# Kernel tuning notes

Measured on AMD Instinct MI355X. Metric: run time of the kernel, lower is better.

Reference implementation:

```python
import jax, jax.numpy as jnp
import numpy as np

DIM = 512
NUM_LATENTS = 512
HIDDEN = 48  # PointEmbed sinusoidal embedding dim (divisible by 6)


def make_basis():
    k = HIDDEN // 6
    e = (2.0 ** np.arange(k)) * np.pi
    z = np.zeros(k)
    basis = np.stack([
        np.concatenate([e, z, z]),
        np.concatenate([z, e, z]),
        np.concatenate([z, z, e]),
    ])  # [3, HIDDEN//2]
    return jnp.asarray(basis, jnp.float32)


def layernorm(x, g, b, eps=1e-5):
    m = x.mean(-1, keepdims=True)
    v = ((x - m) ** 2).mean(-1, keepdims=True)
    return (x - m) / jnp.sqrt(v + eps) * g + b


def point_embed(x, basis, w, b):
    # x: [B, N, 3] -> [B, N, DIM//2]
    proj = jnp.einsum('bnd,de->bne', x, basis)
    feat = jnp.concatenate([jnp.sin(proj), jnp.cos(proj), x], axis=-1)  # [B,N,51]
    return feat @ w + b


def fps_single(points, num_samples):
    # deterministic farthest point sampling starting at index 0; non-differentiable
    pts = jax.lax.stop_gradient(points)
    N = pts.shape[0]

    def body(carry, _):
        dists, last = carry
        d = jnp.sum((pts - pts[last]) ** 2, axis=-1)
        dists = jnp.minimum(dists, d)
        nxt = jnp.argmax(dists).astype(jnp.int32)
        return (dists, nxt), nxt

    init = (jnp.full((N,), 1e10, pts.dtype), jnp.int32(0))
    _, idxs = jax.lax.scan(body, init, None, length=num_samples - 1)
    return jnp.concatenate([jnp.zeros((1,), jnp.int32), idxs])


def setup_inputs() -> dict:
    key = jax.random.key(0)
    ks = jax.random.split(key, 16)
    B, T, N, D = 16, 3, 2048, 3
    s = 0.02
    inp = {
        'pc': jax.random.normal(ks[0], (B, T, N, D), jnp.float32),
        'pc2': jax.random.normal(ks[1], (B, T, N, D), jnp.float32),
        'basis': make_basis(),
        'pe_w': jax.random.normal(ks[2], (HIDDEN + 3, DIM // 2), jnp.float32) * s,
        'pe_b': jnp.zeros((DIM // 2,), jnp.float32),
        'lnq_g': jnp.ones((DIM,), jnp.float32), 'lnq_b': jnp.zeros((DIM,), jnp.float32),
        'lnc_g': jnp.ones((DIM,), jnp.float32), 'lnc_b': jnp.zeros((DIM,), jnp.float32),
        'wq': jax.random.normal(ks[3], (DIM, DIM), jnp.float32) * s,
        'wkv': jax.random.normal(ks[4], (DIM, 2 * DIM), jnp.float32) * s,
        'wo': jax.random.normal(ks[5], (DIM, DIM), jnp.float32) * s,
        'bo': jnp.zeros((DIM,), jnp.float32),
        'lnf_g': jnp.ones((DIM,), jnp.float32), 'lnf_b': jnp.zeros((DIM,), jnp.float32),
        'w1': jax.random.normal(ks[6], (DIM, 8 * DIM), jnp.float32) * s,
        'b1': jnp.zeros((8 * DIM,), jnp.float32),
        'w2': jax.random.normal(ks[7], (4 * DIM, DIM), jnp.float32) * s,
        'b2': jnp.zeros((DIM,), jnp.float32),
    }
    return inp


def reference(pc, pc2, basis, pe_w, pe_b, lnq_g, lnq_b, lnc_g, lnc_b,
              wq, wkv, wo, bo, lnf_g, lnf_b, w1, b1, w2, b2):
    B, T, N, D = pc.shape
    # FPS on the first frame, per batch element (batch-local indices)
    idx = jax.vmap(lambda p: fps_single(p, NUM_LATENTS))(pc[:, 0])  # [B, M]
    idx4 = idx[:, None, :, None]  # broadcast over T and D
    sampled = jnp.take_along_axis(pc, idx4, axis=2).reshape(B * T, NUM_LATENTS, D)
    sampled2 = jnp.take_along_axis(pc2, idx4, axis=2).reshape(B * T, NUM_LATENTS, D)
    pcf = pc.reshape(B * T, N, D)
    pcf2 = pc2.reshape(B * T, N, D)

    emb_s = jnp.concatenate([point_embed(sampled, basis, pe_w, pe_b),
                             point_embed(sampled2, basis, pe_w, pe_b)], axis=-1)
    emb_c = jnp.concatenate([point_embed(pcf, basis, pe_w, pe_b),
                             point_embed(pcf2, basis, pe_w, pe_b)], axis=-1)

    # PreNorm cross-attention (1 head, dim_head = DIM)
    q_in = layernorm(emb_s, lnq_g, lnq_b)
    c_in = layernorm(emb_c, lnc_g, lnc_b)
    q = q_in @ wq
    kv = c_in @ wkv
    k, v = jnp.split(kv, 2, axis=-1)
    scale = DIM ** -0.5
    attn = jax.nn.softmax(jnp.einsum('bmd,bnd->bmn', q, k) * scale, axis=-1)
    out = jnp.einsum('bmn,bnd->bmd', attn, v) @ wo + bo
    x = out + emb_s

    # PreNorm GEGLU feed-forward
    h = layernorm(x, lnf_g, lnf_b) @ w1 + b1
    a, g = jnp.split(h, 2, axis=-1)
    x = (a * jax.nn.gelu(g, approximate=False)) @ w2 + b2 + x

    return x.reshape(B, T, NUM_LATENTS, DIM)
```

## Files before the change

### kernel.cpp

```cpp
#include <hip/hip_runtime.h>

#define NB    16
#define NT    3
#define NCTX  2048
#define NLAT  512
#define DIMV  512
#define HALFD 256
#define NFEAT 51
#define NBT   48
#define MROWS 24576
#define GRP   6
#define NGRP  8
#define GROWS 12288
#define FUSED_BLKS (NB + GROWS/16 + 4096)

typedef unsigned short bfu;
typedef short bf16x8 __attribute__((ext_vector_type(8)));
typedef float f32x4  __attribute__((ext_vector_type(4)));
typedef float f32x2  __attribute__((ext_vector_type(2)));

__device__ __forceinline__ float bf2f(bfu u){ return __uint_as_float(((unsigned int)u) << 16); }
__device__ __forceinline__ bfu f2bf(float f){
  unsigned int u = __float_as_uint(f);
  u += 0x7FFFu + ((u >> 16) & 1u);
  return (bfu)(u >> 16);
}
__device__ __forceinline__ float loadE(const float* p){ return *p; }
__device__ __forceinline__ float loadE(const bfu* p){ return bf2f(*p); }
__device__ __forceinline__ void storeE(float* p, float v){ *p = v; }
__device__ __forceinline__ void storeE(bfu* p, float v){ *p = f2bf(v); }
__device__ __forceinline__ bfu to_bfu(float f){ return f2bf(f); }
__device__ __forceinline__ bfu to_bfu(bfu u){ return u; }

#define GLD16(gp, lp) __builtin_amdgcn_global_load_lds(                       \
    (const __attribute__((address_space(1))) unsigned int*)(gp),              \
    (__attribute__((address_space(3))) unsigned int*)(lp), 16, 0, 0)

template<int KSTEP>
__device__ __forceinline__ int swzr(int r){
  constexpr int CPR = KSTEP / 8;
  return (KSTEP == 32) ? ((r >> 1) & 3) : (r & (CPR - 1));
}

#define DPP_ARGMAX_STAGE(CTRL)                                                \
  {                                                                           \
    const int svb = __builtin_amdgcn_update_dpp(vb, vb, CTRL, 0xF, 0xF, false); \
    const int sib = __builtin_amdgcn_update_dpp(ib, ib, CTRL, 0xF, 0xF, false); \
    const float sv = __int_as_float(svb);                                     \
    const float cv = __int_as_float(vb);                                      \
    if (sv > cv || (sv == cv && sib < ib)){ vb = svb; ib = sib; }             \
  }

__device__ __forceinline__ void fps_body(int b, int tid, const float* __restrict__ pc,
                                         int* __restrict__ idx_out,
                                         float4* pts, int (*mbuf)[4]){
  const int lane = tid & 63, w = tid >> 6;
  const int wbase = w << 10;
  const float* src = pc + (size_t)b * (NT * NCTX * 3);

  f32x2 x2[8], y2[8], z2[8], d2[8];
  #pragma unroll
  for (int j = 0; j < 8; ++j){
    #pragma unroll
    for (int h = 0; h < 2; ++h){
      const int p = wbase + ((2 * j + h) << 6) + lane;
      const float xx = src[p * 3 + 0];
      const float yy = src[p * 3 + 1];
      const float zz = src[p * 3 + 2];
      x2[j][h] = xx; y2[j][h] = yy; z2[j][h] = zz;
      pts[p] = make_float4(xx, yy, zz, 0.f);
    }
    d2[j][0] = 1e10f; d2[j][1] = 1e10f;
  }
  if (tid == 0) idx_out[b * NLAT] = 0;
  __syncthreads();

  int last = 0;
  for (int step = 1; step < NLAT; ++step){
    const float4 lp = pts[last];

    #pragma unroll
    for (int j = 0; j < 8; ++j){
      const f32x2 dx = x2[j] - lp.x;
      const f32x2 dy = y2[j] - lp.y;
      const f32x2 dz = z2[j] - lp.z;
      const f32x2 dd = (dx * dx + dy * dy) + dz * dz;
      f32x2 nd;
      nd[0] = fminf(d2[j][0], dd[0]);
      nd[1] = fminf(d2[j][1], dd[1]);
      d2[j] = nd;
    }

    float av[8]; int as_[8];
    #pragma unroll
    for (int j = 0; j < 8; ++j){
      const float lo = d2[j][0], hi = d2[j][1];
      const bool t = hi > lo;
      av[j]  = t ? hi : lo;
      as_[j] = t ? 2 * j + 1 : 2 * j;
    }
    #pragma unroll
    for (int wdt = 4; wdt; wdt >>= 1){
      #pragma unroll
      for (int j = 0; j < wdt; ++j){
        const float lv = av[2 * j], rv = av[2 * j + 1];
        const int   li = as_[2 * j], ri = as_[2 * j + 1];
        const bool t = rv > lv;
        av[j]  = t ? rv : lv;
        as_[j] = t ? ri : li;
      }
    }

    int vb = __float_as_int(av[0]);
    int ib = wbase + (as_[0] << 6) + lane;
    DPP_ARGMAX_STAGE(0x111)
    DPP_ARGMAX_STAGE(0x112)
    DPP_ARGMAX_STAGE(0x114)
    DPP_ARGMAX_STAGE(0x118)
    DPP_ARGMAX_STAGE(0x142)
    DPP_ARGMAX_STAGE(0x143)

    const int par = step & 1;
    if (lane == 63){ mbuf[par][w * 2] = vb; mbuf[par][w * 2 + 1] = ib; }
    __syncthreads();
    const int4 q = *(const int4*)&mbuf[par][0];
    const float f0 = __int_as_float(q.x), f1 = __int_as_float(q.z);
    last = (f1 > f0) ? q.w : q.y;
    if (tid == 0) idx_out[b * NLAT + step] = last;
  }
}

template<bool GATHER, bool WRITE_EMB>
__device__ __forceinline__ void embed_body(
    int bid, int tid,
    const float* __restrict__ pc, const float* __restrict__ pc2,
    const int* __restrict__ idx,
    const float* __restrict__ basis, const float* __restrict__ pe_w,
    const float* __restrict__ pe_b,
    const float* __restrict__ ln_g, const float* __restrict__ ln_b,
    bfu* __restrict__ emb, bfu* __restrict__ lnout, int nppbt,
    float (*feat)[16][NFEAT + 1], float (*outb)[DIMV])
{
  const int p0 = bid << 4;

  if (tid < 32){
    const int s = tid >> 4, p = tid & 15;
    const int gp = p0 + p;
    const int bt = gp / nppbt;
    const int n  = gp - bt * nppbt;
    const int bb = bt / NT;
    const int srcn = GATHER ? idx[bb * NLAT + n] : n;
    const float* sp = (s ? pc2 : pc) + ((size_t)bt * NCTX + srcn) * 3;
    feat[s][p][48] = sp[0]; feat[s][p][49] = sp[1]; feat[s][p][50] = sp[2];
  }
  __syncthreads();

  #pragma unroll
  for (int t = 0; t < 3; ++t){
    const int wk  = tid * 3 + t;
    const int spq = wk / 24;
    const int e   = wk - spq * 24;
    const int s = spq >> 4, p = spq & 15;
    const float x0 = feat[s][p][48], x1 = feat[s][p][49], x2 = feat[s][p][50];
    const float pr = __fadd_rn(__fadd_rn(__fmul_rn(x0, basis[e]),
                                         __fmul_rn(x1, basis[24 + e])),
                               __fmul_rn(x2, basis[48 + e]));
    feat[s][p][e]      = sinf(pr);
    feat[s][p][24 + e] = cosf(pr);
  }
  __syncthreads();

  {
    float w[NFEAT];
    #pragma unroll
    for (int k = 0; k < NFEAT; ++k) w[k] = pe_w[k * HALFD + tid];
    const float bv = pe_b[tid];
    #pragma unroll
    for (int half = 0; half < 2; ++half){
      for (int p = 0; p < 16; ++p){
        float acc = bv;
        #pragma unroll
        for (int k = 0; k < NFEAT; ++k) acc = fmaf(feat[half][p][k], w[k], acc);
        outb[p][half * HALFD + tid] = acc;
      }
    }
  }
  __syncthreads();

  const int lane = tid & 63, wv = tid >> 6;
  for (int pp = 0; pp < 4; ++pp){
    const int p = (wv << 2) + pp;
    const size_t gp = (size_t)p0 + p;
    float x[8];
    #pragma unroll
    for (int j = 0; j < 8; ++j) x[j] = outb[p][lane + (j << 6)];
    float s = 0.f;
    #pragma unroll
    for (int j = 0; j < 8; ++j) s += x[j];
    for (int o = 32; o; o >>= 1) s += __shfl_xor(s, o, 64);
    const float m = s * (1.0f / 512.0f);
    float s2 = 0.f;
    #pragma unroll
    for (int j = 0; j < 8; ++j){ const float d = x[j] - m; s2 = fmaf(d, d, s2); }
    for (int o = 32; o; o >>= 1) s2 += __shfl_xor(s2, o, 64);
    const float inv = 1.0f / sqrtf(s2 * (1.0f / 512.0f) + 1e-5f);
    #pragma unroll
    for (int j = 0; j < 8; ++j){
      const int c = lane + (j << 6);
      const float r = (x[j] - m) * inv * ln_g[c] + ln_b[c];
      const size_t o2 = gp * DIMV + c;
      if (WRITE_EMB) emb[o2] = f2bf(x[j]);
      lnout[o2] = f2bf(r);
    }
  }
}

template<bool GATHER, bool WRITE_EMB>
__global__ __launch_bounds__(256) void embed_kernel(
    const float* __restrict__ pc, const float* __restrict__ pc2,
    const int* __restrict__ idx,
    const float* __restrict__ basis, const float* __restrict__ pe_w,
    const float* __restrict__ pe_b,
    const float* __restrict__ ln_g, const float* __restrict__ ln_b,
    bfu* __restrict__ emb, bfu* __restrict__ lnout, int nppbt)
{
  __shared__ float feat[2][16][NFEAT + 1];
  __shared__ float outb[16][DIMV];
  embed_body<GATHER, WRITE_EMB>(blockIdx.x, threadIdx.x, pc, pc2, idx, basis,
      pe_w, pe_b, ln_g, ln_b, emb, lnout, nppbt, feat, outb);
}

template<typename TIN>
__device__ __forceinline__ void transp_body(
    const TIN* __restrict__ in, bfu* __restrict__ out, int R, int C,
    int bx, int by, bfu (*t)[33])
{
  const int c0 = bx * 32, r0 = by * 32;
  const int tx = threadIdx.x & 31, ty = threadIdx.x >> 5;
  #pragma unroll
  for (int rr = ty; rr < 32; rr += 8)
    t[rr][tx] = to_bfu(in[(size_t)(r0 + rr) * C + c0 + tx]);
  __syncthreads();
  #pragma unroll
  for (int rr = ty; rr < 32; rr += 8)
    out[(size_t)(c0 + rr) * R + r0 + tx] = t[tx][rr];
}

template<typename TIN>
__global__ __launch_bounds__(256) void transp_kernel(
    const TIN* __restrict__ in, bfu* __restrict__ out, int R, int C,
    long long sIn, long long sOut)
{
  __shared__ bfu t[32][33];
  transp_body<TIN>(in + (size_t)blockIdx.z * sIn, out + (size_t)blockIdx.z * sOut,
                   R, C, blockIdx.x, blockIdx.y, t);
}

__global__ __attribute__((amdgpu_waves_per_eu(1, 1)))
__launch_bounds__(256) void fused_pre(
    const float* __restrict__ pc, const float* __restrict__ pc2,
    int* __restrict__ idx_out,
    const float* __restrict__ basis, const float* __restrict__ pe_w,
    const float* __restrict__ pe_b,
    const float* __restrict__ lnc_g, const float* __restrict__ lnc_b,
    bfu* __restrict__ c_grp,
    const float* __restrict__ wq, const float* __restrict__ wkv,
    const float* __restrict__ wo, const float* __restrict__ w1,
    const float* __restrict__ w2,
    bfu* __restrict__ wqT, bfu* __restrict__ wkvT, bfu* __restrict__ woT,
    bfu* __restrict__ w1T, bfu* __restrict__ w2T)
{
  __shared__ __align__(16) char smem[39424];
  const int bid = blockIdx.x, tid = threadIdx.x;

  if (bid < NB){
    #pragma clang fp contract(off)
    float4* pts = (float4*)smem;
    int (*mbuf)[4] = (int(*)[4])(smem + 32768);
    if (tid < 128){
      fps_body(bid, tid, pc, idx_out, pts, mbuf);
    } else {
      for (int i = 0; i < NLAT; ++i) __syncthreads();
    }
    return;
  }
  const int rb = bid - NB;
  if (rb < GROWS / 16){
    embed_body<false, false>(rb, tid, pc, pc2, nullptr, basis, pe_w, pe_b,
                             lnc_g, lnc_b, nullptr, c_grp, NCTX,
                             (float(*)[16][NFEAT + 1])smem,
                             (float(*)[DIMV])(smem + 6656));
    return;
  }
  int tb = rb - GROWS / 16;
  bfu (*tile)[33] = (bfu(*)[33])smem;
  if (tb < 256){ transp_body<float>(wq,  wqT,  512,  512, tb & 15,  tb >> 4, tile); return; }
  tb -= 256;
  if (tb < 512){ transp_body<float>(wkv, wkvT, 512, 1024, tb & 31,  tb >> 5, tile); return; }
  tb -= 512;
  if (tb < 256){ transp_body<float>(wo,  woT,  512,  512, tb & 15,  tb >> 4, tile); return; }
  tb -= 256;
  if (tb < 2048){ transp_body<float>(w1, w1T,  512, 4096, tb & 127, tb >> 7, tile); return; }
  tb -= 2048;
  transp_body<float>(w2, w2T, 2048, 512, tb & 15, tb >> 4, tile);
}

#define EPI_NONE     0
#define EPI_SPLIT    1
#define EPI_SCALE    2
#define EPI_BIAS_RES 3

template<int FH, int KSTEP, typename TC, typename TR, int EPI>
__global__ __launch_bounds__(256, 2) void gemm_mfma(
    const bfu* __restrict__ A, const bfu* __restrict__ B,
    TC* __restrict__ C, TC* __restrict__ C2,
    const float* __restrict__ bias, const TR* __restrict__ res,
    float scale, int N, int K, int lda, int ldb, int ldc,
    long long sA, long long sB, long long sC)
{
  constexpr int BT  = FH * 32;
  constexpr int CPR = KSTEP / 8;
  constexpr int NI  = (BT * CPR) / 256;
  const int bz = blockIdx.z;
  A += (size_t)bz * sA;
  B += (size_t)bz * sB;
  const size_t coff = (size_t)bz * sC;

  __shared__ __align__(16) short As[BT * KSTEP];
  __shared__ __align__(16) short Bs[BT * KSTEP];

  const int tid = threadIdx.x;
  const int lane = tid & 63, w = tid >> 6;
  const int wl = (w << 6) + lane;
  const int m0 = blockIdx.y * BT, n0 = blockIdx.x * BT;
  const int wm = (w & 1) * (FH * 16), wn = (w >> 1) * (FH * 16);
  const int fr = lane & 15, quad = lane >> 4;

  f32x4 acc[FH][FH];
  #pragma unroll
  for (int i = 0; i < FH; ++i)
    #pragma unroll
    for (int j = 0; j < FH; ++j)
      #pragma unroll
      for (int r = 0; r < 4; ++r) acc[i][j][r] = 0.f;

  for (int k0 = 0; k0 < K; k0 += KSTEP){
    #pragma unroll
    for (int i = 0; i < NI; ++i){
      const int ch = i * 256 + wl;
      const int r  = ch / CPR, cs = ch & (CPR - 1);
      const int cg = cs ^ swzr<KSTEP>(r);
      short* la = (short*)As + ((i * 256 + (w << 6)) << 3);
      short* lb = (short*)Bs + ((i * 256 + (w << 6)) << 3);
      GLD16(A + (size_t)(m0 + r) * lda + k0 + cg * 8, la);
      GLD16(B + (size_t)(n0 + r) * ldb + k0 + cg * 8, lb);
    }
    __syncthreads();
    #pragma unroll
    for (int kk = 0; kk < KSTEP / 32; ++kk){
      bf16x8 af[FH], bf[FH];
      #pragma unroll
      for (int i = 0; i < FH; ++i){
        const int row = wm + i * 16 + fr;
        const int cl = (kk * 4 + quad) ^ swzr<KSTEP>(row);
        af[i] = *(const bf16x8*)&As[row * KSTEP + (cl << 3)];
      }
      #pragma unroll
      for (int j = 0; j < FH; ++j){
        const int row = wn + j * 16 + fr;
        const int cl = (kk * 4 + quad) ^ swzr<KSTEP>(row);
        bf[j] = *(const bf16x8*)&Bs[row * KSTEP + (cl << 3)];
      }
      #pragma unroll
      for (int i = 0; i < FH; ++i)
        #pragma unroll
        for (int j = 0; j < FH; ++j)
          acc[i][j] = __builtin_amdgcn_mfma_f32_16x16x32_bf16(af[i], bf[j], acc[i][j], 0, 0, 0);
    }
    __syncthreads();
  }

  TC* Cp = C + coff;
  #pragma unroll
  for (int i = 0; i < FH; ++i){
    #pragma unroll
    for (int r = 0; r < 4; ++r){
      const int cm = m0 + wm + i * 16 + quad * 4 + r;
      #pragma unroll
      for (int j = 0; j < FH; ++j){
        const int cn = n0 + wn + j * 16 + fr;
        float v = acc[i][j][r];
        if (EPI == EPI_SCALE)    v *= scale;
        if (EPI == EPI_BIAS_RES) v = v + bias[cn] + loadE(&res[coff + (size_t)cm * ldc + cn]);
        if (EPI == EPI_SPLIT){
          const int half = N >> 1;
          if (cn < half) storeE(&C [(size_t)cm * half + cn],          v);
          else           storeE(&C2[(size_t)cm * half + (cn - half)], v);
        } else {
          storeE(&Cp[(size_t)cm * ldc + cn], v);
        }
      }
    }
  }
}

__global__ __launch_bounds__(256, 1) void mlp1_mfma(
    const bfu* __restrict__ A, const bfu* __restrict__ B,
    const float* __restrict__ b1, bfu* __restrict__ act)
{
  constexpr int KSTEP = 64, CPR = 8, NI = 4;
  __shared__ __align__(16) short As[128 * KSTEP];
  __shared__ __align__(16) short Ba[128 * KSTEP];
  __shared__ __align__(16) short Bg[128 * KSTEP];

  const int tid = threadIdx.x;
  const int lane = tid & 63, w = tid >> 6;
  const int wl = (w << 6) + lane;
  const int m0 = blockIdx.y * 128, n0 = blockIdx.x * 128;
  const int wm = (w & 1) * 64, wn = (w >> 1) * 64;
  const int fr = lane & 15, quad = lane >> 4;

  f32x4 acca[4][4], accg[4][4];
  #pragma unroll
  for (int i = 0; i < 4; ++i)
    #pragma unroll
    for (int j = 0; j < 4; ++j)
      #pragma unroll
      for (int r = 0; r < 4; ++r){ acca[i][j][r] = 0.f; accg[i][j][r] = 0.f; }

  for (int k0 = 0; k0 < 512; k0 += KSTEP){
    #pragma unroll
    for (int i = 0; i < NI; ++i){
      const int ch = i * 256 + wl;
      const int r  = ch / CPR, cs = ch & (CPR - 1);
      const int cg = cs ^ swzr<KSTEP>(r);
      short* da = (short*)As + ((i * 256 + (w << 6)) << 3);
      short* db = (short*)Ba + ((i * 256 + (w << 6)) << 3);
      short* dg = (short*)Bg + ((i * 256 + (w << 6)) << 3);
      GLD16(A + (size_t)(m0 + r) * 512 + k0 + cg * 8, da);
      GLD16(B + (size_t)(n0 + r) * 512 + k0 + cg * 8, db);
      GLD16(B + (size_t)(n0 + 2048 + r) * 512 + k0 + cg * 8, dg);
    }
    __syncthreads();
    #pragma unroll
    for (int kk = 0; kk < KSTEP / 32; ++kk){
      bf16x8 af[4], ba[4], bg[4];
      #pragma unroll
      for (int i = 0; i < 4; ++i){
        const int row = wm + i * 16 + fr;
        const int cl = (kk * 4 + quad) ^ swzr<KSTEP>(row);
        af[i] = *(const bf16x8*)&As[row * KSTEP + (cl << 3)];
      }
      #pragma unroll
      for (int j = 0; j < 4; ++j){
        const int row = wn + j * 16 + fr;
        const int cl = (kk * 4 + quad) ^ swzr<KSTEP>(row);
        ba[j] = *(const bf16x8*)&Ba[row * KSTEP + (cl << 3)];
        bg[j] = *(const bf16x8*)&Bg[row * KSTEP + (cl << 3)];
      }
      #pragma unroll
      for (int i = 0; i < 4; ++i)
        #pragma unroll
        for (int j = 0; j < 4; ++j){
          acca[i][j] = __builtin_amdgcn_mfma_f32_16x16x32_bf16(af[i], ba[j], acca[i][j], 0, 0, 0);
          accg[i][j] = __builtin_amdgcn_mfma_f32_16x16x32_bf16(af[i], bg[j], accg[i][j], 0, 0, 0);
        }
    }
    __syncthreads();
  }

  #pragma unroll
  for (int i = 0; i < 4; ++i){
    #pragma unroll
    for (int r = 0; r < 4; ++r){
      const int cm = m0 + wm + i * 16 + quad * 4 + r;
      #pragma unroll
      for (int j = 0; j < 4; ++j){
        const int cn = n0 + wn + j * 16 + fr;
        const float a = acca[i][j][r] + b1[cn];
        const float g = accg[i][j][r] + b1[cn + 2048];
        const float ge = g * 0.5f * (1.0f + erff(g * 0.70710678118654752f));
        act[(size_t)cm * 2048 + cn] = f2bf(a * ge);
      }
    }
  }
}

__global__ __launch_bounds__(256) void softmax_kernel(bfu* __restrict__ sc){
  __shared__ float red[4];
  const int tid = threadIdx.x;
  const int lane = tid & 63, wv = tid >> 6;
  bfu* rp = sc + (size_t)blockIdx.x * NCTX;
  float x[8];
  #pragma unroll
  for (int j = 0; j < 8; ++j) x[j] = bf2f(rp[tid + (j << 8)]);
  float mx = x[0];
  #pragma unroll
  for (int j = 1; j < 8; ++j) mx = fmaxf(mx, x[j]);
  for (int o = 32; o; o >>= 1) mx = fmaxf(mx, __shfl_xor(mx, o, 64));
  if (lane == 0) red[wv] = mx;
  __syncthreads();
  mx = fmaxf(fmaxf(red[0], red[1]), fmaxf(red[2], red[3]));
  float sum = 0.f;
  #pragma unroll
  for (int j = 0; j < 8; ++j){ x[j] = __expf(x[j] - mx); sum += x[j]; }
  for (int o = 32; o; o >>= 1) sum += __shfl_xor(sum, o, 64);
  __syncthreads();
  if (lane == 0) red[wv] = sum;
  __syncthreads();
  sum = red[0] + red[1] + red[2] + red[3];
  const float inv = 1.0f / sum;
  #pragma unroll
  for (int j = 0; j < 8; ++j) rp[tid + (j << 8)] = f2bf(x[j] * inv);
}

__global__ __launch_bounds__(256) void ln_kernel(const float* __restrict__ in,
                                                 const float* __restrict__ g,
                                                 const float* __restrict__ b,
                                                 bfu* __restrict__ out){
  const int tid = threadIdx.x, lane = tid & 63, wv = tid >> 6;
  const size_t row = (size_t)blockIdx.x * 4 + wv;
  const float* rp = in + row * DIMV;
  float x[8];
  #pragma unroll
  for (int j = 0; j < 8; ++j) x[j] = rp[lane + (j << 6)];
  float s = 0.f;
  #pragma unroll
  for (int j = 0; j < 8; ++j) s += x[j];
  for (int o = 32; o; o >>= 1) s += __shfl_xor(s, o, 64);
  const float m = s * (1.0f / 512.0f);
  float s2 = 0.f;
  #pragma unroll
  for (int j = 0; j < 8; ++j){ const float d = x[j] - m; s2 = fmaf(d, d, s2); }
  for (int o = 32; o; o >>= 1) s2 += __shfl_xor(s2, o, 64);
  const float inv = 1.0f / sqrtf(s2 * (1.0f / 512.0f) + 1e-5f);
  bfu* op = out + row * DIMV;
  #pragma unroll
  for (int j = 0; j < 8; ++j){
    const int c = lane + (j << 6);
    op[c] = f2bf((x[j] - m) * inv * g[c] + b[c]);
  }
}

extern "C" void kernel_launch(void* const* d_in, const int* in_sizes, int n_in,
                              void* d_out, int out_size, void* d_ws, size_t ws_size,
                              hipStream_t stream)
{
  (void)in_sizes; (void)n_in; (void)out_size;
  if (ws_size < 121667584ull) return;

  const float* pc    = (const float*)d_in[0];
  const float* pc2   = (const float*)d_in[1];
  const float* basis = (const float*)d_in[2];
  const float* pe_w  = (const float*)d_in[3];
  const float* pe_b  = (const float*)d_in[4];
  const float* lnq_g = (const float*)d_in[5];
  const float* lnq_b = (const float*)d_in[6];
  const float* lnc_g = (const float*)d_in[7];
  const float* lnc_b = (const float*)d_in[8];
  const float* wq    = (const float*)d_in[9];
  const float* wkv   = (const float*)d_in[10];
  const float* wo    = (const float*)d_in[11];
  const float* bo    = (const float*)d_in[12];
  const float* lnf_g = (const float*)d_in[13];
  const float* lnf_b = (const float*)d_in[14];
  const float* w1    = (const float*)d_in[15];
  const float* b1    = (const float*)d_in[16];
  const float* w2    = (const float*)d_in[17];
  const float* b2    = (const float*)d_in[18];
  float* xout = (float*)d_out;

  char* ws = (char*)d_ws;
  int* idxb   = (int*)(ws);
  bfu* emb_s  = (bfu*)(ws + 32768);
  bfu* q_in   = (bfu*)(ws + 25198592);
  bfu* c_grp  = (bfu*)(ws + 50364416);
  bfu* k_grp  = (bfu*)(ws + 62947328);
  bfu* v_grp  = (bfu*)(ws + 75530240);
  bfu* qbuf   = (bfu*)(ws + 88113152);
  bfu* wqT    = (bfu*)(ws + 113278976);
  bfu* wkvT   = (bfu*)(ws + 113803264);
  bfu* woT    = (bfu*)(ws + 114851840);
  bfu* w1T    = (bfu*)(ws + 115376128);
  bfu* w2T    = (bfu*)(ws + 119570432);
  bfu* scores  = c_grp;
  bfu* vT      = k_grp;
  bfu* attnout = q_in;
  bfu* lnx     = qbuf;
  bfu* actb    = emb_s;

  fused_pre<<<FUSED_BLKS, 256, 0, stream>>>(
      pc, pc2, idxb, basis, pe_w, pe_b, lnc_g, lnc_b, c_grp,
      wq, wkv, wo, w1, w2, wqT, wkvT, woT, w1T, w2T);

  embed_kernel<true, true><<<MROWS/16, 256, 0, stream>>>(
      pc, pc2, idxb, basis, pe_w, pe_b, lnq_g, lnq_b, emb_s, q_in, NLAT);

  gemm_mfma<4, 64, bfu, float, EPI_NONE><<<dim3(4, 192, 1), 256, 0, stream>>>(
      q_in, wqT, qbuf, nullptr, nullptr, nullptr, 1.0f,
      512, 512, 512, 512, 512, 0, 0, 0);

  for (int g = 0; g < NGRP; ++g){
    const int bt0 = g * GRP;
    if (g > 0){
      embed_kernel<false, false><<<GROWS/16, 256, 0, stream>>>(
          pc + (size_t)bt0 * NCTX * 3, pc2 + (size_t)bt0 * NCTX * 3, nullptr,
          basis, pe_w, pe_b, lnc_g, lnc_b, nullptr, c_grp, NCTX);
    }

    gemm_mfma<4, 64, bfu, float, EPI_SPLIT><<<dim3(8, 96, 1), 256, 0, stream>>>(
        c_grp, wkvT, k_grp, v_grp, nullptr, nullptr, 1.0f,
        1024, 512, 512, 512, 512, 0, 0, 0);

    gemm_mfma<4, 64, bfu, float, EPI_SCALE><<<dim3(16, 4, GRP), 256, 0, stream>>>(
        qbuf + (size_t)bt0 * 262144, k_grp, scores, nullptr, nullptr, nullptr,
        0.044194173824159216f,
        2048, 512, 512, 512, 2048, 262144, 1048576, 1048576);

    softmax_kernel<<<GRP * 512, 256, 0, stream>>>(scores);

    transp_kernel<bfu><<<dim3(16, 64, GRP), 256, 0, stream>>>(
        v_grp, vT, 2048, 512, 2048*512, 2048*512);

    gemm_mfma<2, 128, bfu, float, EPI_NONE><<<dim3(8, 8, GRP), 256, 0, stream>>>(
        scores, vT, attnout + (size_t)bt0 * 262144, nullptr, nullptr, nullptr, 1.0f,
        512, 2048, 2048, 2048, 512, 1048576, 1048576, 262144);
  }

  gemm_mfma<4, 64, float, bfu, EPI_BIAS_RES><<<dim3(4, 192, 1), 256, 0, stream>>>(
      attnout, woT, xout, nullptr, bo, emb_s, 1.0f,
      512, 512, 512, 512, 512, 0, 0, 0);

  ln_kernel<<<MROWS/4, 256, 0, stream>>>(xout, lnf_g, lnf_b, lnx);

  for (int h = 0; h < 2; ++h){
    const size_t ro = (size_t)h * 12288;
    mlp1_mfma<<<dim3(16, 96, 1), 256, 0, stream>>>(
        lnx + ro * 512, w1T, b1, actb);
    gemm_mfma<4, 64, float, float, EPI_BIAS_RES><<<dim3(4, 96, 1), 256, 0, stream>>>(
        actb, w2T, xout + ro * 512, nullptr, b2, xout + ro * 512, 1.0f,
        512, 2048, 2048, 2048, 512, 0, 0, 0);
  }
}
```

Baseline: 1.703 ms.

## Compute V transposed directly via swapped GEMM and widen FPS to four waves

The V projection is now computed as W_v^T · C^T with a separate GEMM that writes V already transposed, so the per-group transpose kernel is no longer needed. The split KV GEMM becomes a K-only GEMM. Farthest point sampling now uses all four waves of the block, each holding 512 points instead of 1024, with a four-way cross-wave argmax in shared memory. This trades one extra GEMM launch per group for removing a transpose pass over V, and shortens the serial FPS chain, which may overlap other work.

```diff
diff --git a/kernel.cpp b/kernel.cpp
--- a/kernel.cpp
+++ b/kernel.cpp
@@ -53,14 +53,14 @@
 
 __device__ __forceinline__ void fps_body(int b, int tid, const float* __restrict__ pc,
                                          int* __restrict__ idx_out,
-                                         float4* pts, int (*mbuf)[4]){
+                                         float4* pts, int (*mbuf)[8]){
   const int lane = tid & 63, w = tid >> 6;
-  const int wbase = w << 10;
+  const int wbase = w << 9;
   const float* src = pc + (size_t)b * (NT * NCTX * 3);
 
-  f32x2 x2[8], y2[8], z2[8], d2[8];
-  #pragma unroll
-  for (int j = 0; j < 8; ++j){
+  f32x2 x2[4], y2[4], z2[4], d2[4];
+  #pragma unroll
+  for (int j = 0; j < 4; ++j){
     #pragma unroll
     for (int h = 0; h < 2; ++h){
       const int p = wbase + ((2 * j + h) << 6) + lane;
@@ -80,7 +80,7 @@
     const float4 lp = pts[last];
 
     #pragma unroll
-    for (int j = 0; j < 8; ++j){
+    for (int j = 0; j < 4; ++j){
       const f32x2 dx = x2[j] - lp.x;
       const f32x2 dy = y2[j] - lp.y;
       const f32x2 dz = z2[j] - lp.z;
@@ -91,16 +91,16 @@
       d2[j] = nd;
     }
 
-    float av[8]; int as_[8];
-    #pragma unroll
-    for (int j = 0; j < 8; ++j){
+    float av[4]; int as_[4];
+    #pragma unroll
+    for (int j = 0; j < 4; ++j){
       const float lo = d2[j][0], hi = d2[j][1];
       const bool t = hi > lo;
       av[j]  = t ? hi : lo;
       as_[j] = t ? 2 * j + 1 : 2 * j;
     }
     #pragma unroll
-    for (int wdt = 4; wdt; wdt >>= 1){
+    for (int wdt = 2; wdt; wdt >>= 1){
       #pragma unroll
       for (int j = 0; j < wdt; ++j){
         const float lv = av[2 * j], rv = av[2 * j + 1];
@@ -123,9 +123,13 @@
     const int par = step & 1;
     if (lane == 63){ mbuf[par][w * 2] = vb; mbuf[par][w * 2 + 1] = ib; }
     __syncthreads();
-    const int4 q = *(const int4*)&mbuf[par][0];
-    const float f0 = __int_as_float(q.x), f1 = __int_as_float(q.z);
-    last = (f1 > f0) ? q.w : q.y;
+    const int4 q0 = *(const int4*)&mbuf[par][0];
+    const int4 q1 = *(const int4*)&mbuf[par][4];
+    float bv = __int_as_float(q0.x); int bi = q0.y;
+    { const float v1 = __int_as_float(q0.z); if (v1 > bv){ bv = v1; bi = q0.w; } }
+    { const float v2 = __int_as_float(q1.x); if (v2 > bv){ bv = v2; bi = q1.y; } }
+    { const float v3 = __int_as_float(q1.z); if (v3 > bv){ bv = v3; bi = q1.w; } }
+    last = bi;
     if (tid == 0) idx_out[b * NLAT + step] = last;
   }
 }
@@ -244,16 +248,6 @@
   #pragma unroll
   for (int rr = ty; rr < 32; rr += 8)
     out[(size_t)(c0 + rr) * R + r0 + tx] = t[tx][rr];
-}
-
-template<typename TIN>
-__global__ __launch_bounds__(256) void transp_kernel(
-    const TIN* __restrict__ in, bfu* __restrict__ out, int R, int C,
-    long long sIn, long long sOut)
-{
-  __shared__ bfu t[32][33];
-  transp_body<TIN>(in + (size_t)blockIdx.z * sIn, out + (size_t)blockIdx.z * sOut,
-                   R, C, blockIdx.x, blockIdx.y, t);
 }
 
 __global__ __attribute__((amdgpu_waves_per_eu(1, 1)))
@@ -276,12 +270,8 @@
   if (bid < NB){
     #pragma clang fp contract(off)
     float4* pts = (float4*)smem;
-    int (*mbuf)[4] = (int(*)[4])(smem + 32768);
-    if (tid < 128){
-      fps_body(bid, tid, pc, idx_out, pts, mbuf);
-    } else {
-      for (int i = 0; i < NLAT; ++i) __syncthreads();
-    }
+    int (*mbuf)[8] = (int(*)[8])(smem + 32768);
+    fps_body(bid, tid, pc, idx_out, pts, mbuf);
     return;
   }
   const int rb = bid - NB;
@@ -584,7 +574,7 @@
   bfu* w1T    = (bfu*)(ws + 115376128);
   bfu* w2T    = (bfu*)(ws + 119570432);
   bfu* scores  = c_grp;
-  bfu* vT      = k_grp;
+  bfu* vT      = v_grp;
   bfu* attnout = q_in;
   bfu* lnx     = qbuf;
   bfu* actb    = emb_s;
@@ -608,9 +598,13 @@
           basis, pe_w, pe_b, lnc_g, lnc_b, nullptr, c_grp, NCTX);
     }
 
-    gemm_mfma<4, 64, bfu, float, EPI_SPLIT><<<dim3(8, 96, 1), 256, 0, stream>>>(
-        c_grp, wkvT, k_grp, v_grp, nullptr, nullptr, 1.0f,
-        1024, 512, 512, 512, 512, 0, 0, 0);
+    gemm_mfma<4, 64, bfu, float, EPI_NONE><<<dim3(4, 96, 1), 256, 0, stream>>>(
+        c_grp, wkvT, k_grp, nullptr, nullptr, nullptr, 1.0f,
+        512, 512, 512, 512, 512, 0, 0, 0);
+
+    gemm_mfma<4, 64, bfu, float, EPI_NONE><<<dim3(16, 4, GRP), 256, 0, stream>>>(
+        wkvT + 512 * 512, c_grp, v_grp, nullptr, nullptr, nullptr, 1.0f,
+        2048, 512, 512, 512, 2048, 0, 1048576, 1048576);
 
     gemm_mfma<4, 64, bfu, float, EPI_SCALE><<<dim3(16, 4, GRP), 256, 0, stream>>>(
         qbuf + (size_t)bt0 * 262144, k_grp, scores, nullptr, nullptr, nullptr,
@@ -618,9 +612,6 @@
         2048, 512, 512, 512, 2048, 262144, 1048576, 1048576);
 
     softmax_kernel<<<GRP * 512, 256, 0, stream>>>(scores);
-
-    transp_kernel<bfu><<<dim3(16, 64, GRP), 256, 0, stream>>>(
-        v_grp, vT, 2048, 512, 2048*512, 2048*512);
 
     gemm_mfma<2, 128, bfu, float, EPI_NONE><<<dim3(8, 8, GRP), 256, 0, stream>>>(
         scores, vT, attnout + (size_t)bt0 * 262144, nullptr, nullptr, nullptr, 1.0f,
```

Measured after the change: 1.527 ms. 10.3% less time.
